# Optimization experiments

Measured on AMD Instinct MI355X. Metric: run time of the kernel, lower is better.

The kernel has to match this reference:

```python
import jax, jax.numpy as jnp
import numpy as np

TEMP = 0.5  # temperature
UNITS = [512, 256, 128]
B, M, D, C = 256, 512, 512, 8


def setup_inputs() -> dict:
    key = jax.random.key(0)
    ks = jax.random.split(key, 9)
    inp = {}
    inp["ec_output"] = jax.random.normal(ks[0], (B, M, D), jnp.float32)
    inp["mask"] = jax.random.randint(ks[1], (B, 1, 1, M), 0, 2).astype(jnp.float32)
    inp["label"] = jax.random.randint(ks[2], (B, C), 0, 2)
    dims = [D] + UNITS
    for i in range(3):
        fan_in = dims[i]
        inp[f"W{i+1}"] = jax.random.normal(ks[3 + i], (C, dims[i], dims[i + 1]), jnp.float32) * (1.0 / np.sqrt(fan_in))
        inp[f"b{i+1}"] = jnp.zeros((C, dims[i + 1]), jnp.float32)
    return inp


def reference(ec_output, mask, label, W1, b1, W2, b2, W3, b3):
    # masked sum pooling: mask==0 means keep (as in the TF code)
    m = (jnp.squeeze(mask) == 0).astype(ec_output.dtype)  # (B, M)
    pooled = jnp.einsum('bmd,bm->bd', ec_output, m)        # (B, D)

    # per-class 3-layer relu MLP, batched over class axis c
    h = jax.nn.relu(jnp.einsum('bd,cde->cbe', pooled, W1) + b1[:, None, :])
    h = jax.nn.relu(jnp.einsum('cbe,cef->cbf', h, W2) + b2[:, None, :])
    h = jax.nn.relu(jnp.einsum('cbf,cfg->cbg', h, W3) + b3[:, None, :])

    # tf.math.l2_normalize semantics
    z = h * jax.lax.rsqrt(jnp.maximum(jnp.sum(h * h, axis=-1, keepdims=True), 1e-12))  # (C, B, u)

    # supervised contrastive loss per class (training=True path)
    lab = label.T.astype(z.dtype)                 # (C, B)
    mask1 = (lab == 1).astype(z.dtype)
    mask0 = (lab == 0).astype(z.dtype)
    num_p = jnp.sum(mask1, axis=1, keepdims=True)  # (C, 1)
    num_n = jnp.sum(mask0, axis=1, keepdims=True)
    num_vec = num_p * mask1 + num_n * mask0        # (C, B)

    ip = jnp.einsum('cbe,cke->cbk', z, z)          # (C, B, B)
    ip = ip * (1.0 - jnp.eye(B, dtype=z.dtype)) / TEMP

    denom = num_vec * jnp.log(jnp.sum(jnp.exp(ip), axis=2))  # (C, B)
    numer = mask1 * jnp.einsum('cbk,ck->cb', ip, mask1) + mask0 * jnp.einsum('cbk,ck->cb', ip, mask0)
    losses = -jnp.sum((numer - denom) / num_vec, axis=1)      # (C,)

    return z, losses
```

## Files before the change

kernel.cpp:

```cpp
#include <hip/hip_runtime.h>
#include <hip/hip_bf16.h>

typedef unsigned short u16;
typedef __bf16 bf16x8 __attribute__((ext_vector_type(8)));
typedef float f32x4 __attribute__((ext_vector_type(4)));


__device__ __forceinline__ float bf2f(u16 u) {
    union { float f; unsigned int i; } x; x.i = ((unsigned int)u) << 16; return x.f;
}
__device__ __forceinline__ u16 f2bf(float f) {
    union { float f; unsigned int i; } x; x.f = f;
    unsigned int r = x.i + 0x7FFFu + ((x.i >> 16) & 1u);
    return (u16)(r >> 16);
}

__global__ __launch_bounds__(1024) void pool_kernel(
    const u16* __restrict__ ec, const u16* __restrict__ mask,
    u16* __restrict__ pooled)
{
    int b = blockIdx.x, tid = threadIdx.x;
    __shared__ float wm[512];
    __shared__ float red[16][512];
    if (tid < 512)
        wm[tid] = (bf2f(mask[b * 512 + tid]) == 0.0f) ? 1.0f : 0.0f;
    __syncthreads();
    int g = tid & 63, mo = tid >> 6;
    float acc[8];
    #pragma unroll
    for (int j = 0; j < 8; j++) acc[j] = 0.0f;
    const u16* base = ec + (size_t)b * 512 * 512;
    for (int m = mo; m < 512; m += 16) {
        if (wm[m] != 0.0f) {
            union { uint4 v; u16 s[8]; } u;
            u.v = *(const uint4*)&base[(size_t)m * 512 + g * 8];
            #pragma unroll
            for (int j = 0; j < 8; j++) acc[j] += bf2f(u.s[j]);
        }
    }
    #pragma unroll
    for (int j = 0; j < 8; j++) red[mo][g * 8 + j] = acc[j];
    __syncthreads();
    if (tid < 512) {
        float s = 0.0f;
        #pragma unroll
        for (int k = 0; k < 16; k++) s += red[k][tid];
        pooled[(size_t)b * 512 + tid] = f2bf(s);
    }
}

__global__ __launch_bounds__(512) void mlp_gemm64(
    const u16* __restrict__ A, const u16* __restrict__ W,
    const u16* __restrict__ bias, u16* __restrict__ out,
    int K, int N, int aBatch, int mtiles, int ntiles)
{
    int bid = blockIdx.x;
    int per_c = mtiles * ntiles;
    int c = bid / per_c, rem = bid % per_c;
    int mt = rem / ntiles, nt = rem % ntiles;
    const u16* aBase = A + (size_t)c * aBatch + (size_t)mt * 64 * K;
    const u16* wBase = W + (size_t)c * K * N + nt * 64;
    __shared__ __align__(16) u16 As[2][64][72];
    __shared__ __align__(16) u16 Bs[2][64][72];
    int tid = threadIdx.x;
    int w = tid >> 6, l15 = tid & 15, q = (tid >> 4) & 3;
    int wm = w >> 1, wn = w & 1;
    int r0 = tid >> 3, kc0 = tid & 7;
    f32x4 acc[2];
    #pragma unroll
    for (int t = 0; t < 2; t++)
        #pragma unroll
        for (int e = 0; e < 4; e++) acc[t][e] = 0.0f;

    uint4 aReg, wReg;
    aReg = *(const uint4*)&aBase[(size_t)r0 * K + kc0 * 8];
    wReg = *(const uint4*)&wBase[(size_t)r0 * N + kc0 * 8];

    int nIter = K >> 6;
    for (int it = 0; it < nIter; ++it) {
        int cur = it & 1;
        *(uint4*)&As[cur][r0][kc0 * 8] = aReg;
        {
            union { uint4 v; u16 s[8]; } u; u.v = wReg;
            #pragma unroll
            for (int j = 0; j < 8; j++) Bs[cur][kc0 * 8 + j][r0] = u.s[j];
        }
        if (it + 1 < nIter) {
            int k0n = (it + 1) * 64;
            aReg = *(const uint4*)&aBase[(size_t)r0 * K + k0n + kc0 * 8];
            wReg = *(const uint4*)&wBase[(size_t)(k0n + r0) * N + kc0 * 8];
        }
        __syncthreads();
        #pragma unroll
        for (int ks = 0; ks < 64; ks += 32) {
            bf16x8 av = *(const bf16x8*)&As[cur][wm * 16 + l15][ks + q * 8];
            #pragma unroll
            for (int t = 0; t < 2; t++) {
                bf16x8 bv = *(const bf16x8*)&Bs[cur][wn * 32 + t * 16 + l15][ks + q * 8];
                acc[t] = __builtin_amdgcn_mfma_f32_16x16x32_bf16(av, bv, acc[t], 0, 0, 0);
            }
        }
    }
    #pragma unroll
    for (int t = 0; t < 2; t++) {
        int col = nt * 64 + wn * 32 + t * 16 + l15;
        float bv = bf2f(bias[c * N + col]);
        #pragma unroll
        for (int r = 0; r < 4; r++) {
            int row = mt * 64 + wm * 16 + q * 4 + r;
            float v = acc[t][r] + bv;
            v = v > 0.0f ? v : 0.0f;
            out[((size_t)c * 256 + row) * N + col] = f2bf(v);
        }
    }
}

__global__ __launch_bounds__(256) void mlp_gemm3_norm(
    const u16* __restrict__ A, const u16* __restrict__ W,
    const u16* __restrict__ bias, float* __restrict__ zout, u16* __restrict__ zbf)
{
    const int K = 256, N = 128;
    int bid = blockIdx.x;
    int c = bid >> 4, mt = bid & 15;
    const u16* aBase = A + ((size_t)c * 256 + mt * 16) * K;
    const u16* wBase = W + (size_t)c * K * N;
    __shared__ __align__(16) u16 As[16][72];
    __shared__ __align__(16) u16 Bs[128][72];
    __shared__ float ssq_s[4][16];
    __shared__ float scale_s[16];
    int tid = threadIdx.x;
    int w = tid >> 6, l15 = tid & 15, q = (tid >> 4) & 3;
    f32x4 acc[2];
    #pragma unroll
    for (int t = 0; t < 2; t++)
        #pragma unroll
        for (int e = 0; e < 4; e++) acc[t][e] = 0.0f;

    for (int k0 = 0; k0 < K; k0 += 64) {
        if (tid < 128) {
            int r = tid >> 3, kc = tid & 7;
            *(uint4*)&As[r][kc * 8] = *(const uint4*)&aBase[(size_t)r * K + k0 + kc * 8];
        }
        #pragma unroll
        for (int i = 0; i < 4; i++) {
            int idx = tid + i * 256;
            int kk = idx >> 4, n8 = (idx & 15) * 8;
            union { uint4 v; u16 s[8]; } u;
            u.v = *(const uint4*)&wBase[(size_t)(k0 + kk) * N + n8];
            #pragma unroll
            for (int j = 0; j < 8; j++) Bs[n8 + j][kk] = u.s[j];
        }
        __syncthreads();
        #pragma unroll
        for (int ks = 0; ks < 64; ks += 32) {
            bf16x8 av = *(const bf16x8*)&As[l15][ks + q * 8];
            #pragma unroll
            for (int t = 0; t < 2; t++) {
                bf16x8 bv = *(const bf16x8*)&Bs[w * 32 + t * 16 + l15][ks + q * 8];
                acc[t] = __builtin_amdgcn_mfma_f32_16x16x32_bf16(av, bv, acc[t], 0, 0, 0);
            }
        }
        __syncthreads();
    }
    float val[2][4];
    float ssq[4] = {0.f, 0.f, 0.f, 0.f};
    #pragma unroll
    for (int t = 0; t < 2; t++) {
        float bv = bf2f(bias[c * N + w * 32 + t * 16 + l15]);
        #pragma unroll
        for (int r = 0; r < 4; r++) {
            float v = acc[t][r] + bv;
            v = v > 0.0f ? v : 0.0f;
            val[t][r] = v;
            ssq[r] += v * v;
        }
    }
    #pragma unroll
    for (int off = 1; off < 16; off <<= 1)
        #pragma unroll
        for (int r = 0; r < 4; r++) ssq[r] += __shfl_xor(ssq[r], off);
    if (l15 == 0) {
        #pragma unroll
        for (int r = 0; r < 4; r++) ssq_s[w][q * 4 + r] = ssq[r];
    }
    __syncthreads();
    if (tid < 16) {
        float s = ssq_s[0][tid] + ssq_s[1][tid] + ssq_s[2][tid] + ssq_s[3][tid];
        scale_s[tid] = rsqrtf(fmaxf(s, 1e-12f));
    }
    __syncthreads();
    #pragma unroll
    for (int t = 0; t < 2; t++)
        #pragma unroll
        for (int r = 0; r < 4; r++) {
            int row = mt * 16 + q * 4 + r;
            int col = w * 32 + t * 16 + l15;
            float zv = val[t][r] * scale_s[q * 4 + r];
            size_t o = ((size_t)c * 256 + row) * 128 + col;
            zout[o] = zv;
            zbf[o] = f2bf(zv);
        }
}

__global__ __launch_bounds__(1024) void contrast_loss(
    const u16* __restrict__ z, const int* __restrict__ label,
    float* __restrict__ losses)
{
    int c = blockIdx.x;
    int tid = threadIdx.x;
    int w = tid >> 6, l15 = tid & 15, q = (tid >> 4) & 3;
    int rw = w >> 2, cw = w & 3;
    __shared__ __align__(16) u16 Zk[256][136];
    __shared__ float lm1[256];
    __shared__ float npw[16];
    __shared__ float pr_s[4][256];
    __shared__ float p1_s[4][256];
    __shared__ float p0_s[4][256];
    __shared__ float term_s[256];
    __shared__ float red4[4];

    const u16* zc = z + (size_t)c * 256 * 128;
    #pragma unroll
    for (int i = 0; i < 4; i++) {
        int idx = tid + i * 1024;
        int r = idx >> 4, kc = idx & 15;
        *(uint4*)&Zk[r][kc * 8] = *(const uint4*)&zc[(size_t)r * 128 + kc * 8];
    }
    float m1 = 0.0f;
    if (tid < 256) {
        m1 = (label[tid * 8 + c] == 1) ? 1.0f : 0.0f;
        lm1[tid] = m1;
    }
    float nps = m1;
    #pragma unroll
    for (int off = 1; off < 64; off <<= 1) nps += __shfl_xor(nps, off);
    if ((tid & 63) == 0) npw[w] = nps;
    __syncthreads();

    f32x4 acc[4][4];
    #pragma unroll
    for (int a = 0; a < 4; a++)
        #pragma unroll
        for (int t = 0; t < 4; t++)
            #pragma unroll
            for (int e = 0; e < 4; e++) acc[a][t][e] = 0.0f;
    #pragma unroll
    for (int ks = 0; ks < 128; ks += 32) {
        bf16x8 av[4], bv[4];
        #pragma unroll
        for (int a = 0; a < 4; a++)
            av[a] = *(const bf16x8*)&Zk[rw * 64 + a * 16 + l15][ks + q * 8];
        #pragma unroll
        for (int t = 0; t < 4; t++)
            bv[t] = *(const bf16x8*)&Zk[cw * 64 + t * 16 + l15][ks + q * 8];
        #pragma unroll
        for (int a = 0; a < 4; a++)
            #pragma unroll
            for (int t = 0; t < 4; t++)
                acc[a][t] = __builtin_amdgcn_mfma_f32_16x16x32_bf16(av[a], bv[t], acc[a][t], 0, 0, 0);
    }
    #pragma unroll
    for (int a = 0; a < 4; a++) {
        float pr[4] = {0.f, 0.f, 0.f, 0.f};
        float p1[4] = {0.f, 0.f, 0.f, 0.f};
        float p0[4] = {0.f, 0.f, 0.f, 0.f};
        #pragma unroll
        for (int t = 0; t < 4; t++) {
            int kbg = cw * 64 + t * 16 + l15;
            float mm = lm1[kbg];
            #pragma unroll
            for (int r = 0; r < 4; r++) {
                int rbg = rw * 64 + a * 16 + q * 4 + r;
                float v = (rbg == kbg) ? 0.0f : acc[a][t][r] * 2.0f;
                pr[r] += __expf(v);
                p1[r] += v * mm;
                p0[r] += v * (1.0f - mm);
            }
        }
        #pragma unroll
        for (int off = 1; off < 16; off <<= 1)
            #pragma unroll
            for (int r = 0; r < 4; r++) {
                pr[r] += __shfl_xor(pr[r], off);
                p1[r] += __shfl_xor(p1[r], off);
                p0[r] += __shfl_xor(p0[r], off);
            }
        if (l15 == 0) {
            #pragma unroll
            for (int r = 0; r < 4; r++) {
                int rbg = rw * 64 + a * 16 + q * 4 + r;
                pr_s[cw][rbg] = pr[r];
                p1_s[cw][rbg] = p1[r];
                p0_s[cw][rbg] = p0[r];
            }
        }
    }
    __syncthreads();
    if (tid < 256) {
        float rt = pr_s[0][tid] + pr_s[1][tid] + pr_s[2][tid] + pr_s[3][tid];
        float s1 = p1_s[0][tid] + p1_s[1][tid] + p1_s[2][tid] + p1_s[3][tid];
        float s0 = p0_s[0][tid] + p0_s[1][tid] + p0_s[2][tid] + p0_s[3][tid];
        float np = 0.0f;
        #pragma unroll
        for (int k = 0; k < 16; k++) np += npw[k];
        float m = lm1[tid];
        float num_vec = (m > 0.0f) ? np : 256.0f - np;
        float numer = (m > 0.0f) ? s1 : s0;
        term_s[tid] = numer / num_vec - __logf(rt);
    }
    __syncthreads();
    if (tid < 256) {
        float t4 = term_s[tid];
        #pragma unroll
        for (int off = 1; off < 64; off <<= 1) t4 += __shfl_xor(t4, off);
        if ((tid & 63) == 0) red4[w] = t4;
    }
    __syncthreads();
    if (tid == 0) losses[c] = -(red4[0] + red4[1] + red4[2] + red4[3]);
}

extern "C" void kernel_launch(void* const* d_in, const int* in_sizes, int n_in,
                              void* d_out, int out_size, void* d_ws, size_t ws_size,
                              hipStream_t stream) {
    (void)in_sizes; (void)n_in; (void)ws_size;
    const u16* ec   = (const u16*)d_in[0];
    const u16* mask = (const u16*)d_in[1];
    const int* label = (const int*)d_in[2];
    const u16* W1 = (const u16*)d_in[3];
    const u16* b1 = (const u16*)d_in[4];
    const u16* W2 = (const u16*)d_in[5];
    const u16* b2 = (const u16*)d_in[6];
    const u16* W3 = (const u16*)d_in[7];
    const u16* b3 = (const u16*)d_in[8];
    float* zout = (float*)d_out;
    char* ws = (char*)d_ws;
    u16* pooled = (u16*)(ws + 0);
    u16* h1     = (u16*)(ws + 262144);
    u16* h2     = (u16*)(ws + 2359296);
    u16* zbf    = (u16*)(ws + 3407872);

    pool_kernel<<<256, 1024, 0, stream>>>(ec, mask, pooled);
    mlp_gemm64<<<256, 512, 0, stream>>>(pooled, W1, b1, h1, 512, 512, 0, 4, 8);
    mlp_gemm64<<<128, 512, 0, stream>>>(h1, W2, b2, h2, 512, 256, 256 * 512, 4, 4);
    mlp_gemm3_norm<<<128, 256, 0, stream>>>(h2, W3, b3, zout, zbf);
    contrast_loss<<<8, 1024, 0, stream>>>(zbf, label, zout + (out_size - 8));
}
```

Measured before the change: 380.6 us.

## Fuse third MLP layer and L2 norm into contrastive loss kernel

```diff
diff --git a/kernel.cpp b/kernel.cpp
--- a/kernel.cpp
+++ b/kernel.cpp
@@ -115,117 +115,33 @@
     }
 }
 
-__global__ __launch_bounds__(256) void mlp_gemm3_norm(
+__global__ __launch_bounds__(1024) void mlp3_contrast(
     const u16* __restrict__ A, const u16* __restrict__ W,
-    const u16* __restrict__ bias, float* __restrict__ zout, u16* __restrict__ zbf)
+    const u16* __restrict__ bias, const int* __restrict__ label,
+    float* __restrict__ zout, float* __restrict__ losses)
 {
     const int K = 256, N = 128;
-    int bid = blockIdx.x;
-    int c = bid >> 4, mt = bid & 15;
-    const u16* aBase = A + ((size_t)c * 256 + mt * 16) * K;
-    const u16* wBase = W + (size_t)c * K * N;
-    __shared__ __align__(16) u16 As[16][72];
-    __shared__ __align__(16) u16 Bs[128][72];
-    __shared__ float ssq_s[4][16];
-    __shared__ float scale_s[16];
-    int tid = threadIdx.x;
-    int w = tid >> 6, l15 = tid & 15, q = (tid >> 4) & 3;
-    f32x4 acc[2];
-    #pragma unroll
-    for (int t = 0; t < 2; t++)
-        #pragma unroll
-        for (int e = 0; e < 4; e++) acc[t][e] = 0.0f;
-
-    for (int k0 = 0; k0 < K; k0 += 64) {
-        if (tid < 128) {
-            int r = tid >> 3, kc = tid & 7;
-            *(uint4*)&As[r][kc * 8] = *(const uint4*)&aBase[(size_t)r * K + k0 + kc * 8];
-        }
-        #pragma unroll
-        for (int i = 0; i < 4; i++) {
-            int idx = tid + i * 256;
-            int kk = idx >> 4, n8 = (idx & 15) * 8;
-            union { uint4 v; u16 s[8]; } u;
-            u.v = *(const uint4*)&wBase[(size_t)(k0 + kk) * N + n8];
-            #pragma unroll
-            for (int j = 0; j < 8; j++) Bs[n8 + j][kk] = u.s[j];
-        }
-        __syncthreads();
-        #pragma unroll
-        for (int ks = 0; ks < 64; ks += 32) {
-            bf16x8 av = *(const bf16x8*)&As[l15][ks + q * 8];
-            #pragma unroll
-            for (int t = 0; t < 2; t++) {
-                bf16x8 bv = *(const bf16x8*)&Bs[w * 32 + t * 16 + l15][ks + q * 8];
-                acc[t] = __builtin_amdgcn_mfma_f32_16x16x32_bf16(av, bv, acc[t], 0, 0, 0);
-            }
-        }
-        __syncthreads();
-    }
-    float val[2][4];
-    float ssq[4] = {0.f, 0.f, 0.f, 0.f};
-    #pragma unroll
-    for (int t = 0; t < 2; t++) {
-        float bv = bf2f(bias[c * N + w * 32 + t * 16 + l15]);
-        #pragma unroll
-        for (int r = 0; r < 4; r++) {
-            float v = acc[t][r] + bv;
-            v = v > 0.0f ? v : 0.0f;
-            val[t][r] = v;
-            ssq[r] += v * v;
-        }
-    }
-    #pragma unroll
-    for (int off = 1; off < 16; off <<= 1)
-        #pragma unroll
-        for (int r = 0; r < 4; r++) ssq[r] += __shfl_xor(ssq[r], off);
-    if (l15 == 0) {
-        #pragma unroll
-        for (int r = 0; r < 4; r++) ssq_s[w][q * 4 + r] = ssq[r];
-    }
-    __syncthreads();
-    if (tid < 16) {
-        float s = ssq_s[0][tid] + ssq_s[1][tid] + ssq_s[2][tid] + ssq_s[3][tid];
-        scale_s[tid] = rsqrtf(fmaxf(s, 1e-12f));
-    }
-    __syncthreads();
-    #pragma unroll
-    for (int t = 0; t < 2; t++)
-        #pragma unroll
-        for (int r = 0; r < 4; r++) {
-            int row = mt * 16 + q * 4 + r;
-            int col = w * 32 + t * 16 + l15;
-            float zv = val[t][r] * scale_s[q * 4 + r];
-            size_t o = ((size_t)c * 256 + row) * 128 + col;
-            zout[o] = zv;
-            zbf[o] = f2bf(zv);
-        }
-}
-
-__global__ __launch_bounds__(1024) void contrast_loss(
-    const u16* __restrict__ z, const int* __restrict__ label,
-    float* __restrict__ losses)
-{
     int c = blockIdx.x;
     int tid = threadIdx.x;
     int w = tid >> 6, l15 = tid & 15, q = (tid >> 4) & 3;
     int rw = w >> 2, cw = w & 3;
+
+    __shared__ __align__(16) u16 As[256][72];
+    __shared__ __align__(16) u16 Bs[128][72];
     __shared__ __align__(16) u16 Zk[256][136];
     __shared__ float lm1[256];
     __shared__ float npw[16];
+    __shared__ float ssq_s[4][256];
+    __shared__ float scale_s[256];
     __shared__ float pr_s[4][256];
     __shared__ float p1_s[4][256];
     __shared__ float p0_s[4][256];
     __shared__ float term_s[256];
     __shared__ float red4[4];
 
-    const u16* zc = z + (size_t)c * 256 * 128;
-    #pragma unroll
-    for (int i = 0; i < 4; i++) {
-        int idx = tid + i * 1024;
-        int r = idx >> 4, kc = idx & 15;
-        *(uint4*)&Zk[r][kc * 8] = *(const uint4*)&zc[(size_t)r * 128 + kc * 8];
-    }
+    const u16* aBase = A + (size_t)c * 256 * K;
+    const u16* wBase = W + (size_t)c * K * N;
+
     float m1 = 0.0f;
     if (tid < 256) {
         m1 = (label[tid * 8 + c] == 1) ? 1.0f : 0.0f;
@@ -235,6 +151,95 @@
     #pragma unroll
     for (int off = 1; off < 64; off <<= 1) nps += __shfl_xor(nps, off);
     if ((tid & 63) == 0) npw[w] = nps;
+
+    f32x4 g[4][2];
+    #pragma unroll
+    for (int a = 0; a < 4; a++)
+        #pragma unroll
+        for (int t = 0; t < 2; t++)
+            #pragma unroll
+            for (int e = 0; e < 4; e++) g[a][t][e] = 0.0f;
+
+    for (int k0 = 0; k0 < K; k0 += 64) {
+        #pragma unroll
+        for (int i = 0; i < 2; i++) {
+            int idx = tid + i * 1024;
+            int r = idx >> 3, kc = idx & 7;
+            *(uint4*)&As[r][kc * 8] = *(const uint4*)&aBase[(size_t)r * K + k0 + kc * 8];
+        }
+        {
+            int kk = tid >> 4, n8 = (tid & 15) * 8;
+            union { uint4 v; u16 s[8]; } u;
+            u.v = *(const uint4*)&wBase[(size_t)(k0 + kk) * N + n8];
+            #pragma unroll
+            for (int j = 0; j < 8; j++) Bs[n8 + j][kk] = u.s[j];
+        }
+        __syncthreads();
+        #pragma unroll
+        for (int ks = 0; ks < 64; ks += 32) {
+            bf16x8 av[4];
+            #pragma unroll
+            for (int a = 0; a < 4; a++)
+                av[a] = *(const bf16x8*)&As[rw * 64 + a * 16 + l15][ks + q * 8];
+            #pragma unroll
+            for (int t = 0; t < 2; t++) {
+                bf16x8 bv = *(const bf16x8*)&Bs[cw * 32 + t * 16 + l15][ks + q * 8];
+                #pragma unroll
+                for (int a = 0; a < 4; a++)
+                    g[a][t] = __builtin_amdgcn_mfma_f32_16x16x32_bf16(av[a], bv, g[a][t], 0, 0, 0);
+            }
+        }
+        __syncthreads();
+    }
+
+    float ssqa[4][4];
+    #pragma unroll
+    for (int a = 0; a < 4; a++)
+        #pragma unroll
+        for (int r = 0; r < 4; r++) ssqa[a][r] = 0.0f;
+    #pragma unroll
+    for (int t = 0; t < 2; t++) {
+        float bv = bf2f(bias[c * N + cw * 32 + t * 16 + l15]);
+        #pragma unroll
+        for (int a = 0; a < 4; a++)
+            #pragma unroll
+            for (int r = 0; r < 4; r++) {
+                float v = g[a][t][r] + bv;
+                v = v > 0.0f ? v : 0.0f;
+                g[a][t][r] = v;
+                ssqa[a][r] += v * v;
+            }
+    }
+    #pragma unroll
+    for (int off = 1; off < 16; off <<= 1)
+        #pragma unroll
+        for (int a = 0; a < 4; a++)
+            #pragma unroll
+            for (int r = 0; r < 4; r++) ssqa[a][r] += __shfl_xor(ssqa[a][r], off);
+    if (l15 == 0) {
+        #pragma unroll
+        for (int a = 0; a < 4; a++)
+            #pragma unroll
+            for (int r = 0; r < 4; r++)
+                ssq_s[cw][rw * 64 + a * 16 + q * 4 + r] = ssqa[a][r];
+    }
+    __syncthreads();
+    if (tid < 256)
+        scale_s[tid] = rsqrtf(fmaxf(
+            ssq_s[0][tid] + ssq_s[1][tid] + ssq_s[2][tid] + ssq_s[3][tid], 1e-12f));
+    __syncthreads();
+    #pragma unroll
+    for (int a = 0; a < 4; a++)
+        #pragma unroll
+        for (int t = 0; t < 2; t++)
+            #pragma unroll
+            for (int r = 0; r < 4; r++) {
+                int row = rw * 64 + a * 16 + q * 4 + r;
+                int col = cw * 32 + t * 16 + l15;
+                float zv = g[a][t][r] * scale_s[row];
+                Zk[row][col] = f2bf(zv);
+                zout[((size_t)c * 256 + row) * 128 + col] = zv;
+            }
     __syncthreads();
 
     f32x4 acc[4][4];
@@ -337,11 +342,9 @@
     u16* pooled = (u16*)(ws + 0);
     u16* h1     = (u16*)(ws + 262144);
     u16* h2     = (u16*)(ws + 2359296);
-    u16* zbf    = (u16*)(ws + 3407872);
 
     pool_kernel<<<256, 1024, 0, stream>>>(ec, mask, pooled);
     mlp_gemm64<<<256, 512, 0, stream>>>(pooled, W1, b1, h1, 512, 512, 0, 4, 8);
     mlp_gemm64<<<128, 512, 0, stream>>>(h1, W2, b2, h2, 512, 256, 256 * 512, 4, 4);
-    mlp_gemm3_norm<<<128, 256, 0, stream>>>(h2, W3, b3, zout, zbf);
-    contrast_loss<<<8, 1024, 0, stream>>>(zbf, label, zout + (out_size - 8));
-}
+    mlp3_contrast<<<8, 1024, 0, stream>>>(h2, W3, b3, label, zout, zout + (out_size - 8));
+}
```

Result: no change. 385.1 us (+1.2%).
